# Kernel tuning notes

Hardware: AMD Instinct MI355X
Metric: run time of the kernel (lower is better)

## Reference

```python
import jax, jax.numpy as jnp
import numpy as np
from functools import partial

D_MODEL = 768
N_LAYER = 2
VOCAB = 50264  # 50257 padded to multiple of 8
D_STATE = 16
D_INNER = 2 * D_MODEL
DT_RANK = 48
D_CONV = 4
EPS = 1e-5
ZOH_EPS = 1e-7
B, L = 2, 1024


def setup_inputs() -> dict:
    key = jax.random.key(0)
    ks = jax.random.split(key, 16)
    s = 0.02
    inp = {
        'input_ids': jax.random.randint(ks[0], (B, L), 0, VOCAB, dtype=jnp.int32),
        'embedding': jax.random.normal(ks[1], (VOCAB, D_MODEL), jnp.float32) * s,
        'in_w': jax.random.normal(ks[2], (N_LAYER, D_MODEL, 2 * D_INNER), jnp.float32) * s,
        'in_b': jnp.zeros((N_LAYER, 2 * D_INNER), jnp.float32),
        'conv_w': jax.random.normal(ks[3], (N_LAYER, D_INNER, D_CONV), jnp.float32) * s,
        'conv_b': jnp.zeros((N_LAYER, D_INNER), jnp.float32),
        'xproj_w': jax.random.normal(ks[4], (N_LAYER, D_INNER, DT_RANK + 2 * D_STATE), jnp.float32) * s,
        'dt_w': jax.random.normal(ks[5], (N_LAYER, DT_RANK, D_INNER), jnp.float32) * s,
        'dt_b': jnp.zeros((N_LAYER, D_INNER), jnp.float32),
        'A_log': jnp.broadcast_to(jnp.log(jnp.arange(1, D_STATE + 1, dtype=jnp.float32))[None, None, :], (N_LAYER, D_INNER, D_STATE)).copy(),
        'Dp': jnp.ones((N_LAYER, D_INNER), jnp.float32),
        'out_w': jax.random.normal(ks[6], (N_LAYER, D_INNER, D_MODEL), jnp.float32) * s,
        'out_b': jnp.zeros((N_LAYER, D_MODEL), jnp.float32),
        'norm_w': jnp.ones((N_LAYER, D_MODEL), jnp.float32),
        'normf_w': jnp.ones((D_MODEL,), jnp.float32),
    }
    return inp


def rmsnorm(x, w):
    return x * jax.lax.rsqrt(jnp.mean(x * x, axis=-1, keepdims=True) + EPS) * w


def mamba_block(x, in_w, in_b, conv_w, conv_b, xproj_w, dt_w, dt_b, A_log, Dp, out_w, out_b):
    # x: (b, l, d_model)
    xr = x @ in_w + in_b                       # (b, l, 2*d_inner)
    xi, res = jnp.split(xr, 2, axis=-1)        # each (b, l, d_inner)
    # causal depthwise conv1d (torch pads d_conv-1 both sides then truncates to l)
    xc = jnp.transpose(xi, (0, 2, 1))          # (b, d_inner, l)
    xc = jax.lax.conv_general_dilated(
        xc, conv_w[:, None, :], (1,), [(D_CONV - 1, 0)],
        dimension_numbers=('NCH', 'OIH', 'NCH'), feature_group_count=D_INNER)
    xc = xc + conv_b[None, :, None]
    u = jax.nn.silu(jnp.transpose(xc, (0, 2, 1)))  # (b, l, d_inner)
    res = jax.nn.silu(res)
    # generate time-varying SSM params
    dbc = u @ xproj_w                          # (b, l, dt_rank + 2n)
    dt, Bm, Cm = jnp.split(dbc, [DT_RANK, DT_RANK + D_STATE], axis=-1)
    delta = jax.nn.softplus(dt @ dt_w + dt_b)  # (b, l, d_inner)
    A = -jnp.exp(A_log)                        # (d_inner, n)
    # ZOH discretization
    dA = jnp.exp(jnp.einsum('bld,dn->bldn', delta, A))            # (b,l,d_in,n)
    zoh = (dA - 1.0) / (A + ZOH_EPS)                               # (b,l,d_in,n)
    dBu = zoh * Bm[:, :, None, :] * u[..., None]                   # (b,l,d_in,n)
    # selective scan over l
    def step(s, inputs):
        dA_t, dBu_t, C_t = inputs              # (b,d_in,n),(b,d_in,n),(b,n)
        s = dA_t * s + dBu_t
        y = jnp.einsum('bdn,bn->bd', s, C_t)
        return s, y
    s0 = jnp.zeros((u.shape[0], D_INNER, D_STATE), u.dtype)
    _, ys = jax.lax.scan(step, s0, (jnp.moveaxis(dA, 1, 0), jnp.moveaxis(dBu, 1, 0), jnp.moveaxis(Cm, 1, 0)))
    y = jnp.moveaxis(ys, 0, 1) + u * Dp        # (b, l, d_inner)
    y = y * res
    return y @ out_w + out_b


def forward(input_ids, embedding, in_w, in_b, conv_w, conv_b, xproj_w, dt_w, dt_b, A_log, Dp, out_w, out_b, norm_w, normf_w):
    x = embedding[input_ids]                   # (b, l, d_model)
    for i in range(N_LAYER):
        mixed = mamba_block(x, in_w[i], in_b[i], conv_w[i], conv_b[i], xproj_w[i],
                            dt_w[i], dt_b[i], A_log[i], Dp[i], out_w[i], out_b[i])
        x = rmsnorm(mixed + x, norm_w[i])      # ResidualBlock: norm(mixer(x)+x)
    x = rmsnorm(x, normf_w)
    return x @ embedding.T                     # tied lm_head, (b, l, vocab)


def reference(input_ids, embedding, in_w, in_b, conv_w, conv_b, xproj_w, dt_w, dt_b, A_log, Dp, out_w, out_b, norm_w, normf_w):
    return forward(input_ids, embedding, in_w, in_b, conv_w, conv_b, xproj_w,
                   dt_w, dt_b, A_log, Dp, out_w, out_b, norm_w, normf_w)
```

## Files before the change

### kernel.cpp

```cpp
#include <hip/hip_runtime.h>
#include <math.h>
#include <stdint.h>

#define BB 2
#define LL 1024
#define DM 768
#define NL 2
#define VV 50264
#define VPAD 50304
#define DS 16
#define DI 1536
#define DR 48
#define DC 4
#define MM (BB*LL)

#define CH 32
#define NC (LL/CH)

#define KS 8

#define TS 64
#define KT 16

typedef __attribute__((ext_vector_type(8))) short short8;
typedef __attribute__((ext_vector_type(4))) float f32x4;

#define AS3(p) ((__attribute__((address_space(3))) unsigned int*)(unsigned int)(uintptr_t)(p))
#define AS1(p) ((const __attribute__((address_space(1))) unsigned int*)(uintptr_t)(p))

__device__ __forceinline__ unsigned short f2bf(float v) {
    union { float f; unsigned u; } x; x.f = v;
    unsigned r = x.u + 0x7fffu + ((x.u >> 16) & 1u);
    return (unsigned short)(r >> 16);
}

__global__ __launch_bounds__(256) void embed_kernel(
    const int* __restrict__ ids, const float* __restrict__ emb,
    float* __restrict__ x, unsigned short* __restrict__ x16)
{
    int m = blockIdx.x;
    int v = ids[m];
    const float* src = emb + (size_t)v * DM;
    float* dst = x + (size_t)m * DM;
    unsigned short* dst16 = x16 + (size_t)m * DM;
    for (int i = threadIdx.x; i < DM; i += 256) {
        float f = src[i];
        dst[i] = f;
        dst16[i] = f2bf(f);
    }
}

__global__ __launch_bounds__(256) void emb_convert_kernel(
    const float* __restrict__ emb, unsigned short* __restrict__ out)
{
    size_t i8 = (size_t)blockIdx.x * 256 + threadIdx.x;
    size_t row = i8 / 96;
    size_t col8 = (i8 - row * 96) * 8;
    if (row >= VPAD) return;
    ushort4 o0, o1;
    if (row < VV) {
        const float* p = emb + row * DM + col8;
        float4 v0 = *(const float4*)p;
        float4 v1 = *(const float4*)(p + 4);
        o0.x = f2bf(v0.x); o0.y = f2bf(v0.y); o0.z = f2bf(v0.z); o0.w = f2bf(v0.w);
        o1.x = f2bf(v1.x); o1.y = f2bf(v1.y); o1.z = f2bf(v1.z); o1.w = f2bf(v1.w);
    } else {
        o0 = make_ushort4(0, 0, 0, 0);
        o1 = o0;
    }
    unsigned short* op = out + row * DM + col8;
    *(ushort4*)op = o0;
    *(ushort4*)(op + 4) = o1;
}

__global__ __launch_bounds__(256) void transpose_bf16_kernel(
    const float* __restrict__ in, unsigned short* __restrict__ out, int R, int C)
{
    __shared__ float t[32][33];
    int l = blockIdx.z;
    int r0 = blockIdx.y * 32, c0 = blockIdx.x * 32;
    int tx = threadIdx.x & 31, ty = threadIdx.x >> 5;
    const float* ip = in + (size_t)l * R * C;
    unsigned short* op = out + (size_t)l * C * R;
    #pragma unroll
    for (int j = 0; j < 32; j += 8)
        t[ty + j][tx] = ip[(size_t)(r0 + ty + j) * C + c0 + tx];
    __syncthreads();
    #pragma unroll
    for (int j = 0; j < 32; j += 8)
        op[(size_t)(c0 + ty + j) * R + r0 + tx] = f2bf(t[tx][ty + j]);
}

__global__ __launch_bounds__(256) void gemm_mfma_bt(
    const unsigned short* __restrict__ A, const unsigned short* __restrict__ B,
    const float* __restrict__ bias, const float* __restrict__ resid,
    float* __restrict__ C, int M, int N, int K, int MT, int NTILES)
{
    int T = MT * NTILES;
    int q = T >> 3, r = T & 7;
    int orig = blockIdx.x;
    int xcd = orig & 7, u = orig >> 3;
    int wg = (xcd < r ? xcd * (q + 1) : r * (q + 1) + (xcd - r) * q) + u;
    int mt = wg % MT, nt = wg / MT;

    __shared__ unsigned short As[3][128 * 32];
    __shared__ unsigned short Bs[3][128 * 32];
    int tid = threadIdx.x;
    int w = tid >> 6, lane = tid & 63;
    int m0 = mt * 128, n0 = nt * 128;

    int rA = lane >> 2;
    int kb = (lane & 3) * 8;
    const unsigned short* gA0 = A + (size_t)(m0 + w * 16 + rA) * K + kb;
    const unsigned short* gA1 = gA0 + (size_t)64 * K;
    const unsigned short* gB0 = B + (size_t)(n0 + w * 16 + rA) * K + kb;
    const unsigned short* gB1 = gB0 + (size_t)64 * K;

    int lr = lane & 15, lk = lane >> 4;
    int wr = (w >> 1) * 64, wc = (w & 1) * 64;

    f32x4 acc[4][4] = {};

#define STAGE(k0, buf) do { \
    __builtin_amdgcn_global_load_lds(AS1(gA0 + (k0)), AS3(&As[buf][(w * 16) * 32]), 16, 0, 0); \
    __builtin_amdgcn_global_load_lds(AS1(gA1 + (k0)), AS3(&As[buf][(64 + w * 16) * 32]), 16, 0, 0); \
    __builtin_amdgcn_global_load_lds(AS1(gB0 + (k0)), AS3(&Bs[buf][(w * 16) * 32]), 16, 0, 0); \
    __builtin_amdgcn_global_load_lds(AS1(gB1 + (k0)), AS3(&Bs[buf][(64 + w * 16) * 32]), 16, 0, 0); \
} while (0)

#define COMPUTE(buf) do { \
    short8 a[4], b[4]; \
    _Pragma("unroll") \
    for (int f = 0; f < 4; ++f) \
        a[f] = *(const short8*)&As[buf][(wr + f * 16 + lr) * 32 + lk * 8]; \
    _Pragma("unroll") \
    for (int f = 0; f < 4; ++f) \
        b[f] = *(const short8*)&Bs[buf][(wc + f * 16 + lr) * 32 + lk * 8]; \
    _Pragma("unroll") \
    for (int i = 0; i < 4; ++i) \
        _Pragma("unroll") \
        for (int j = 0; j < 4; ++j) \
            acc[i][j] = __builtin_amdgcn_mfma_f32_16x16x32_bf16(a[i], b[j], acc[i][j], 0, 0, 0); \
} while (0)

    int nsteps = K / 32;
    STAGE(0, 0);
    STAGE(32, 1);
    asm volatile("s_waitcnt vmcnt(4)" ::: "memory");
    __builtin_amdgcn_s_barrier();
    __builtin_amdgcn_sched_barrier(0);

    for (int t = 0; t < nsteps; ++t) {
        int cur = t % 3;
        if (t + 2 < nsteps)
            STAGE((t + 2) * 32, (t + 2) % 3);
        COMPUTE(cur);
        if (t + 1 < nsteps) {
            if (t + 2 < nsteps)
                asm volatile("s_waitcnt vmcnt(4)" ::: "memory");
            else
                asm volatile("s_waitcnt vmcnt(0)" ::: "memory");
            __builtin_amdgcn_s_barrier();
            __builtin_amdgcn_sched_barrier(0);
        }
    }

#undef STAGE
#undef COMPUTE

    #pragma unroll
    for (int i = 0; i < 4; ++i) {
        int row = m0 + wr + i * 16 + lk * 4;
        #pragma unroll
        for (int j = 0; j < 4; ++j) {
            int col = n0 + wc + j * 16 + lr;
            if (col < N) {
                float bv = bias ? bias[col] : 0.f;
                #pragma unroll
                for (int r2 = 0; r2 < 4; ++r2) {
                    float v = acc[i][j][r2] + bv;
                    if (resid) v += resid[(size_t)(row + r2) * N + col];
                    C[(size_t)(row + r2) * N + col] = v;
                }
            }
        }
    }
}

template<int ACT>
__global__ __launch_bounds__(256) void gemm_tiled(
    const float* __restrict__ A, const float* __restrict__ Bm,
    const float* __restrict__ bias, float* __restrict__ C,
    int M, int N, int K, int lda)
{
    __shared__ float As[KT][TS + 4];
    __shared__ float Bs[KT][TS + 4];
    int tid = threadIdx.x;
    int tx = tid & 15, ty = tid >> 4;
    int m0 = blockIdx.y * TS;
    int n0 = blockIdx.x * TS;
    float acc[4][4] = {};

    for (int k0 = 0; k0 < K; k0 += KT) {
        {
            int i = tid >> 2;
            int k4 = (tid & 3) * 4;
            int m = m0 + i;
            float4 v = make_float4(0.f, 0.f, 0.f, 0.f);
            if (m < M) v = *(const float4*)(A + (size_t)m * lda + k0 + k4);
            As[k4 + 0][i] = v.x; As[k4 + 1][i] = v.y;
            As[k4 + 2][i] = v.z; As[k4 + 3][i] = v.w;
        }
        {
            int k = tid >> 4;
            int j4 = (tid & 15) * 4;
            int n = n0 + j4;
            float4 v = make_float4(0.f, 0.f, 0.f, 0.f);
            const float* p = Bm + (size_t)(k0 + k) * N + n;
            if (n + 3 < N) {
                v = *(const float4*)p;
            } else {
                float t0 = (n + 0 < N) ? p[0] : 0.f;
                float t1 = (n + 1 < N) ? p[1] : 0.f;
                float t2 = (n + 2 < N) ? p[2] : 0.f;
                float t3 = (n + 3 < N) ? p[3] : 0.f;
                v = make_float4(t0, t1, t2, t3);
            }
            Bs[k][j4 + 0] = v.x; Bs[k][j4 + 1] = v.y;
            Bs[k][j4 + 2] = v.z; Bs[k][j4 + 3] = v.w;
        }
        __syncthreads();
        #pragma unroll
        for (int k = 0; k < KT; ++k) {
            float a[4], b[4];
            #pragma unroll
            for (int q2 = 0; q2 < 4; ++q2) a[q2] = As[k][ty * 4 + q2];
            #pragma unroll
            for (int q2 = 0; q2 < 4; ++q2) b[q2] = Bs[k][tx * 4 + q2];
            #pragma unroll
            for (int i = 0; i < 4; ++i)
                #pragma unroll
                for (int j = 0; j < 4; ++j)
                    acc[i][j] = fmaf(a[i], b[j], acc[i][j]);
        }
        __syncthreads();
    }

    #pragma unroll
    for (int i = 0; i < 4; ++i) {
        int m = m0 + ty * 4 + i;
        if (m >= M) continue;
        #pragma unroll
        for (int j = 0; j < 4; ++j) {
            int n = n0 + tx * 4 + j;
            if (n >= N) continue;
            float v = acc[i][j];
            if (bias)  v += bias[n];
            if (ACT == 1) v = fmaxf(v, 0.f) + log1pf(expf(-fabsf(v)));
            C[(size_t)m * N + n] = v;
        }
    }
}

__global__ __launch_bounds__(256) void xproj_part_kernel(
    const float* __restrict__ A, const float* __restrict__ Bm, float* __restrict__ part)
{
    __shared__ float As[KT][TS + 4];
    __shared__ float Bs[KT][TS + 4];
    int tid = threadIdx.x;
    int tx = tid & 15, ty = tid >> 4;
    int m0 = blockIdx.y * TS;
    int n0 = blockIdx.x * TS;
    int kbeg = blockIdx.z * (DI / KS);
    const int N = 80;
    float acc[4][4] = {};

    for (int k0 = kbeg; k0 < kbeg + DI / KS; k0 += KT) {
        {
            int i = tid >> 2;
            int k4 = (tid & 3) * 4;
            float4 v = *(const float4*)(A + (size_t)(m0 + i) * DI + k0 + k4);
            As[k4 + 0][i] = v.x; As[k4 + 1][i] = v.y;
            As[k4 + 2][i] = v.z; As[k4 + 3][i] = v.w;
        }
        {
            int k = tid >> 4;
            int j4 = (tid & 15) * 4;
            int n = n0 + j4;
            const float* p = Bm + (size_t)(k0 + k) * N + n;
            float4 v;
            if (n + 3 < N) {
                v = *(const float4*)p;
            } else {
                v.x = (n + 0 < N) ? p[0] : 0.f;
                v.y = (n + 1 < N) ? p[1] : 0.f;
                v.z = (n + 2 < N) ? p[2] : 0.f;
                v.w = (n + 3 < N) ? p[3] : 0.f;
            }
            Bs[k][j4 + 0] = v.x; Bs[k][j4 + 1] = v.y;
            Bs[k][j4 + 2] = v.z; Bs[k][j4 + 3] = v.w;
        }
        __syncthreads();
        #pragma unroll
        for (int k = 0; k < KT; ++k) {
            float a[4], b[4];
            #pragma unroll
            for (int q2 = 0; q2 < 4; ++q2) a[q2] = As[k][ty * 4 + q2];
            #pragma unroll
            for (int q2 = 0; q2 < 4; ++q2) b[q2] = Bs[k][tx * 4 + q2];
            #pragma unroll
            for (int i = 0; i < 4; ++i)
                #pragma unroll
                for (int j = 0; j < 4; ++j)
                    acc[i][j] = fmaf(a[i], b[j], acc[i][j]);
        }
        __syncthreads();
    }

    float* op = part + (size_t)blockIdx.z * MM * 80;
    #pragma unroll
    for (int i = 0; i < 4; ++i) {
        int m = m0 + ty * 4 + i;
        #pragma unroll
        for (int j = 0; j < 4; ++j) {
            int n = n0 + tx * 4 + j;
            if (n < 80) op[(size_t)m * 80 + n] = acc[i][j];
        }
    }
}

__global__ __launch_bounds__(256) void xproj_reduce_kernel(
    const float* __restrict__ part, float* __restrict__ dbc)
{
    int i = blockIdx.x * 256 + threadIdx.x;
    if (i >= MM * 80) return;
    float s = 0.f;
    #pragma unroll
    for (int z = 0; z < KS; ++z) s += part[(size_t)z * MM * 80 + i];
    dbc[i] = s;
}

__global__ __launch_bounds__(256) void conv_silu_kernel(
    const float* __restrict__ xr, const float* __restrict__ cw,
    const float* __restrict__ cb, float* __restrict__ u)
{
    int d = blockIdx.x * 256 + threadIdx.x;
    int l = blockIdx.y;
    int b = blockIdx.z;
    float acc = cb[d];
    #pragma unroll
    for (int j = 0; j < DC; ++j) {
        int lp = l - (DC - 1) + j;
        if (lp >= 0)
            acc = fmaf(xr[((size_t)(b * LL + lp)) * (2 * DI) + d], cw[d * DC + j], acc);
    }
    float s = acc / (1.f + expf(-acc));
    u[((size_t)(b * LL + l)) * DI + d] = s;
}

__global__ __launch_bounds__(256) void scan_reduce_kernel(
    const float* __restrict__ delta, const float* __restrict__ u,
    const float* __restrict__ dbc, const float* __restrict__ A_log,
    float* __restrict__ P, float* __restrict__ Q)
{
    int d = blockIdx.x * 256 + threadIdx.x;
    int c = blockIdx.y;
    int b = blockIdx.z;

    float Av[DS], invA[DS];
    {
        const float4* ap = (const float4*)(A_log + (size_t)d * DS);
        #pragma unroll
        for (int n4 = 0; n4 < 4; ++n4) {
            float4 a = ap[n4];
            Av[n4 * 4 + 0] = -expf(a.x); Av[n4 * 4 + 1] = -expf(a.y);
            Av[n4 * 4 + 2] = -expf(a.z); Av[n4 * 4 + 3] = -expf(a.w);
        }
        #pragma unroll
        for (int n = 0; n < DS; ++n) invA[n] = 1.f / (Av[n] + 1e-7f);
    }

    float p[DS], s[DS];
    #pragma unroll
    for (int n = 0; n < DS; ++n) { p[n] = 1.f; s[n] = 0.f; }

    const float* dp = delta + ((size_t)b * LL + c * CH) * DI + d;
    const float* up = u     + ((size_t)b * LL + c * CH) * DI + d;
    const float* bb = dbc   + ((size_t)b * LL + c * CH) * 80 + DR;

    for (int l = 0; l < CH; ++l) {
        float dlt = dp[(size_t)l * DI];
        float uv  = up[(size_t)l * DI];
        float Bv[DS];
        {
            const float4* bp4 = (const float4*)(bb + (size_t)l * 80);
            #pragma unroll
            for (int n4 = 0; n4 < 4; ++n4) {
                float4 v = bp4[n4];
                Bv[n4 * 4 + 0] = v.x; Bv[n4 * 4 + 1] = v.y;
                Bv[n4 * 4 + 2] = v.z; Bv[n4 * 4 + 3] = v.w;
            }
        }
        #pragma unroll
        for (int n = 0; n < DS; ++n) {
            float dA = expf(dlt * Av[n]);
            float dBu = (dA - 1.f) * invA[n] * Bv[n] * uv;
            p[n] *= dA;
            s[n] = fmaf(dA, s[n], dBu);
        }
    }

    float* Pp = P + (((size_t)b * NC + c) * DI + d) * DS;
    float* Qp = Q + (((size_t)b * NC + c) * DI + d) * DS;
    #pragma unroll
    for (int n4 = 0; n4 < 4; ++n4) {
        ((float4*)Pp)[n4] = make_float4(p[n4 * 4 + 0], p[n4 * 4 + 1], p[n4 * 4 + 2], p[n4 * 4 + 3]);
        ((float4*)Qp)[n4] = make_float4(s[n4 * 4 + 0], s[n4 * 4 + 1], s[n4 * 4 + 2], s[n4 * 4 + 3]);
    }
}

__global__ __launch_bounds__(256) void scan_apply_kernel(
    const float* __restrict__ delta, const float* __restrict__ u,
    const float* __restrict__ dbc, const float* __restrict__ xr,
    const float* __restrict__ A_log, const float* __restrict__ Dp,
    const float* __restrict__ P, const float* __restrict__ Q,
    unsigned short* __restrict__ y16)
{
    int d = blockIdx.x * 256 + threadIdx.x;
    int c = blockIdx.y;
    int b = blockIdx.z;

    float Av[DS], invA[DS];
    {
        const float4* ap = (const float4*)(A_log + (size_t)d * DS);
        #pragma unroll
        for (int n4 = 0; n4 < 4; ++n4) {
            float4 a = ap[n4];
            Av[n4 * 4 + 0] = -expf(a.x); Av[n4 * 4 + 1] = -expf(a.y);
            Av[n4 * 4 + 2] = -expf(a.z); Av[n4 * 4 + 3] = -expf(a.w);
        }
        #pragma unroll
        for (int n = 0; n < DS; ++n) invA[n] = 1.f / (Av[n] + 1e-7f);
    }
    float Dv = Dp[d];

    float s[DS];
    #pragma unroll
    for (int n = 0; n < DS; ++n) s[n] = 0.f;
    for (int cc = 0; cc < c; ++cc) {
        const float* Pp = P + (((size_t)b * NC + cc) * DI + d) * DS;
        const float* Qp = Q + (((size_t)b * NC + cc) * DI + d) * DS;
        float pv[DS], qv[DS];
        #pragma unroll
        for (int n4 = 0; n4 < 4; ++n4) {
            float4 pw = ((const float4*)Pp)[n4];
            float4 qw = ((const float4*)Qp)[n4];
            pv[n4 * 4 + 0] = pw.x; pv[n4 * 4 + 1] = pw.y; pv[n4 * 4 + 2] = pw.z; pv[n4 * 4 + 3] = pw.w;
            qv[n4 * 4 + 0] = qw.x; qv[n4 * 4 + 1] = qw.y; qv[n4 * 4 + 2] = qw.z; qv[n4 * 4 + 3] = qw.w;
        }
        #pragma unroll
        for (int n = 0; n < DS; ++n) s[n] = fmaf(pv[n], s[n], qv[n]);
    }

    const float* dp = delta + ((size_t)b * LL + c * CH) * DI + d;
    const float* up = u     + ((size_t)b * LL + c * CH) * DI + d;
    const float* xp = xr    + ((size_t)b * LL + c * CH) * (2 * DI) + DI + d;
    const float* bb = dbc   + ((size_t)b * LL + c * CH) * 80 + DR;
    unsigned short* yp = y16 + ((size_t)b * LL + c * CH) * DI + d;

    for (int l = 0; l < CH; ++l) {
        float dlt = dp[(size_t)l * DI];
        float uv  = up[(size_t)l * DI];
        float rv  = xp[(size_t)l * (2 * DI)];
        float Bv[DS], Cv[DS];
        {
            const float4* bp4 = (const float4*)(bb + (size_t)l * 80);
            #pragma unroll
            for (int n4 = 0; n4 < 4; ++n4) {
                float4 v = bp4[n4];
                Bv[n4 * 4 + 0] = v.x; Bv[n4 * 4 + 1] = v.y;
                Bv[n4 * 4 + 2] = v.z; Bv[n4 * 4 + 3] = v.w;
            }
            #pragma unroll
            for (int n4 = 0; n4 < 4; ++n4) {
                float4 v = bp4[4 + n4];
                Cv[n4 * 4 + 0] = v.x; Cv[n4 * 4 + 1] = v.y;
                Cv[n4 * 4 + 2] = v.z; Cv[n4 * 4 + 3] = v.w;
            }
        }
        float pv = 0.f;
        #pragma unroll
        for (int n = 0; n < DS; ++n) {
            float dA = expf(dlt * Av[n]);
            float dBu = (dA - 1.f) * invA[n] * Bv[n] * uv;
            s[n] = fmaf(dA, s[n], dBu);
            pv = fmaf(s[n], Cv[n], pv);
        }
        float res = rv / (1.f + expf(-rv));
        yp[(size_t)l * DI] = f2bf((pv + uv * Dv) * res);
    }
}

__global__ __launch_bounds__(256) void rmsnorm_kernel(
    const float* __restrict__ in, const float* __restrict__ w,
    float* __restrict__ outf, unsigned short* __restrict__ outb)
{
    int m = blockIdx.x;
    const float* row = in + (size_t)m * DM;
    float ss = 0.f;
    for (int i = threadIdx.x; i < DM; i += 256) { float v = row[i]; ss = fmaf(v, v, ss); }
    #pragma unroll
    for (int off = 32; off > 0; off >>= 1) ss += __shfl_down(ss, off);
    __shared__ float sred[4];
    __shared__ float sscale;
    int wid = threadIdx.x >> 6;
    if ((threadIdx.x & 63) == 0) sred[wid] = ss;
    __syncthreads();
    if (threadIdx.x == 0) {
        float tot = sred[0] + sred[1] + sred[2] + sred[3];
        sscale = 1.f / sqrtf(tot / (float)DM + 1e-5f);
    }
    __syncthreads();
    float sc = sscale;
    for (int i = threadIdx.x; i < DM; i += 256) {
        float v = row[i] * sc * w[i];
        if (outf) outf[(size_t)m * DM + i] = v;
        if (outb) outb[(size_t)m * DM + i] = f2bf(v);
    }
}

extern "C" void kernel_launch(void* const* d_in, const int* in_sizes, int n_in,
                              void* d_out, int out_size, void* d_ws, size_t ws_size,
                              hipStream_t stream)
{
    const int*   ids      = (const int*)  d_in[0];
    const float* emb      = (const float*)d_in[1];
    const float* in_w     = (const float*)d_in[2];
    const float* in_b     = (const float*)d_in[3];
    const float* conv_w   = (const float*)d_in[4];
    const float* conv_b   = (const float*)d_in[5];
    const float* xproj_w  = (const float*)d_in[6];
    const float* dt_w     = (const float*)d_in[7];
    const float* dt_b     = (const float*)d_in[8];
    const float* A_log    = (const float*)d_in[9];
    const float* Dp       = (const float*)d_in[10];
    const float* out_w    = (const float*)d_in[11];
    const float* out_b    = (const float*)d_in[12];
    const float* norm_w   = (const float*)d_in[13];
    const float* normf_w  = (const float*)d_in[14];
    float* out = (float*)d_out;

    char* wsp = (char*)d_ws;
    auto alloc = [&](size_t bytes) {
        char* p = wsp;
        wsp += (bytes + 255) & ~(size_t)255;
        return p;
    };
    float* x     = (float*)alloc((size_t)MM * DM * 4);
    float* xr    = (float*)alloc((size_t)MM * 2 * DI * 4);
    float* u     = (float*)alloc((size_t)MM * DI * 4);
    float* dbc   = (float*)alloc((size_t)MM * 80 * 4);
    float* part  = (float*)alloc((size_t)KS * MM * 80 * 4);
    float* delta = (float*)alloc((size_t)MM * DI * 4);
    float* tmp   = (float*)alloc((size_t)MM * DM * 4);
    float* Pbuf  = (float*)alloc((size_t)BB * NC * DI * DS * 4);
    float* Qbuf  = (float*)alloc((size_t)BB * NC * DI * DS * 4);
    unsigned short* x16     = (unsigned short*)alloc((size_t)MM * DM * 2);
    unsigned short* y16     = (unsigned short*)alloc((size_t)MM * DI * 2);
    unsigned short* emb16   = (unsigned short*)alloc((size_t)VPAD * DM * 2);
    unsigned short* in_wT   = (unsigned short*)alloc((size_t)NL * 2 * DI * DM * 2);
    unsigned short* out_wT  = (unsigned short*)alloc((size_t)NL * DM * DI * 2);

    emb_convert_kernel<<<(VPAD * (DM / 8) + 255) / 256, 256, 0, stream>>>(emb, emb16);
    transpose_bf16_kernel<<<dim3(2 * DI / 32, DM / 32, NL), 256, 0, stream>>>(
        in_w, in_wT, DM, 2 * DI);
    transpose_bf16_kernel<<<dim3(DM / 32, DI / 32, NL), 256, 0, stream>>>(
        out_w, out_wT, DI, DM);

    embed_kernel<<<MM, 256, 0, stream>>>(ids, emb, x, x16);

    for (int layer = 0; layer < NL; ++layer) {
        const float* lb_in  = in_b    + (size_t)layer * 2 * DI;
        const float* lcw    = conv_w  + (size_t)layer * DI * DC;
        const float* lcb    = conv_b  + (size_t)layer * DI;
        const float* lxw    = xproj_w + (size_t)layer * DI * (DR + 2 * DS);
        const float* ldtw   = dt_w    + (size_t)layer * DR * DI;
        const float* ldtb   = dt_b    + (size_t)layer * DI;
        const float* lAlog  = A_log   + (size_t)layer * DI * DS;
        const float* lDp    = Dp      + (size_t)layer * DI;
        const float* lob    = out_b   + (size_t)layer * DM;
        const float* lnw    = norm_w  + (size_t)layer * DM;
        const unsigned short* lw_inT = in_wT  + (size_t)layer * 2 * DI * DM;
        const unsigned short* lw_outT= out_wT + (size_t)layer * DM * DI;

        gemm_mfma_bt<<<16 * 24, 256, 0, stream>>>(
            x16, lw_inT, lb_in, nullptr, xr, MM, 2 * DI, DM, 16, 24);

        conv_silu_kernel<<<dim3(DI / 256, LL, BB), 256, 0, stream>>>(xr, lcw, lcb, u);

        xproj_part_kernel<<<dim3(2, MM / TS, KS), 256, 0, stream>>>(u, lxw, part);
        xproj_reduce_kernel<<<(MM * 80 + 255) / 256, 256, 0, stream>>>(part, dbc);

        gemm_tiled<1><<<dim3(DI / TS, MM / TS), 256, 0, stream>>>(
            dbc, ldtw, ldtb, delta, MM, DI, DR, DR + 2 * DS);

        scan_reduce_kernel<<<dim3(DI / 256, NC, BB), 256, 0, stream>>>(
            delta, u, dbc, lAlog, Pbuf, Qbuf);
        scan_apply_kernel<<<dim3(DI / 256, NC, BB), 256, 0, stream>>>(
            delta, u, dbc, xr, lAlog, lDp, Pbuf, Qbuf, y16);

        gemm_mfma_bt<<<16 * 6, 256, 0, stream>>>(
            y16, lw_outT, lob, x, tmp, MM, DM, DI, 16, 6);

        rmsnorm_kernel<<<MM, 256, 0, stream>>>(tmp, lnw, x, x16);
    }

    rmsnorm_kernel<<<MM, 256, 0, stream>>>(x, normf_w, nullptr, x16);

    gemm_mfma_bt<<<16 * (VPAD / 128), 256, 0, stream>>>(
        x16, emb16, nullptr, nullptr, out, MM, VV, DM, 16, VPAD / 128);
}
```

Before: 861.8 us.

## Use a 256x256-tile triple-buffered MFMA GEMM for the tied LM head

Adds a dedicated bf16 MFMA GEMM for the vocabulary projection. It uses 256x256 output tiles, 512 threads, triple-buffered direct global-to-LDS loads, split A/B staging interleaved with compute, XCD-aware block remapping and raised scheduling priority around the MFMAs. The vocabulary padding grows to a multiple of 256 to fit the larger tile. The aim is more data reuse per loaded byte and better overlap in the dominant logits GEMM. In exchange the kernel uses more LDS and registers, which may lower occupancy, and the padded tile count increases slightly.

```diff
diff --git a/kernel.cpp b/kernel.cpp
--- a/kernel.cpp
+++ b/kernel.cpp
@@ -7,7 +7,7 @@
 #define DM 768
 #define NL 2
 #define VV 50264
-#define VPAD 50304
+#define VP2 50432
 #define DS 16
 #define DI 1536
 #define DR 48
@@ -56,7 +56,7 @@
     size_t i8 = (size_t)blockIdx.x * 256 + threadIdx.x;
     size_t row = i8 / 96;
     size_t col8 = (i8 - row * 96) * 8;
-    if (row >= VPAD) return;
+    if (row >= VP2) return;
     ushort4 o0, o1;
     if (row < VV) {
         const float* p = emb + row * DM + col8;
@@ -182,6 +182,121 @@
                     if (resid) v += resid[(size_t)(row + r2) * N + col];
                     C[(size_t)(row + r2) * N + col] = v;
                 }
+            }
+        }
+    }
+}
+
+__global__ __launch_bounds__(512) void gemm_mfma_256(
+    const unsigned short* __restrict__ A, const unsigned short* __restrict__ B,
+    float* __restrict__ C, int M, int N, int K, int MT, int NTILES)
+{
+    int T = MT * NTILES;
+    int q = T >> 3, r = T & 7;
+    int orig = blockIdx.x;
+    int xcd = orig & 7, u = orig >> 3;
+    int wg = (xcd < r ? xcd * (q + 1) : r * (q + 1) + (xcd - r) * q) + u;
+    int mt = wg % MT, nt = wg / MT;
+
+    __shared__ unsigned short As[3][256 * 32];
+    __shared__ unsigned short Bs[3][256 * 32];
+    int tid = threadIdx.x;
+    int w = tid >> 6, lane = tid & 63;
+    int wm = w >> 2, wn = w & 3;
+    int m0 = mt * 256, n0 = nt * 256;
+
+    int srow = tid >> 2;
+    int schunk = (tid & 3) ^ ((srow & 3) ^ ((srow >> 2) & 3));
+    const unsigned short* gA0 = A + (size_t)(m0 + srow) * K + schunk * 8;
+    const unsigned short* gA1 = gA0 + (size_t)128 * K;
+    const unsigned short* gB0 = B + (size_t)(n0 + srow) * K + schunk * 8;
+    const unsigned short* gB1 = gB0 + (size_t)128 * K;
+
+    int lr = lane & 15, lk = lane >> 4;
+    int rc = (lk ^ ((lr & 3) ^ ((lr >> 2) & 3))) * 8;
+
+    f32x4 acc[8][4] = {};
+
+#define STAGE_A(k0, buf) do { \
+    __builtin_amdgcn_global_load_lds(AS1(gA0 + (k0)), AS3(&As[buf][(w * 16) * 32]), 16, 0, 0); \
+    __builtin_amdgcn_global_load_lds(AS1(gA1 + (k0)), AS3(&As[buf][(128 + w * 16) * 32]), 16, 0, 0); \
+} while (0)
+#define STAGE_B(k0, buf) do { \
+    __builtin_amdgcn_global_load_lds(AS1(gB0 + (k0)), AS3(&Bs[buf][(w * 16) * 32]), 16, 0, 0); \
+    __builtin_amdgcn_global_load_lds(AS1(gB1 + (k0)), AS3(&Bs[buf][(128 + w * 16) * 32]), 16, 0, 0); \
+} while (0)
+
+    int nsteps = K / 32;
+
+    STAGE_A(0, 0); STAGE_B(0, 0);
+    STAGE_A(32, 1); STAGE_B(32, 1);
+    asm volatile("s_waitcnt vmcnt(4)" ::: "memory");
+    __builtin_amdgcn_s_barrier();
+    __builtin_amdgcn_sched_barrier(0);
+
+    for (int t = 0; t < nsteps; ++t) {
+        int s = t % 3;
+        int sn = (t + 2) % 3;
+        bool stage2 = (t + 2) < nsteps;
+        short8 av[4], bv[4];
+
+        #pragma unroll
+        for (int f = 0; f < 4; ++f)
+            av[f] = *(const short8*)&As[s][(wm * 128 + f * 16 + lr) * 32 + rc];
+        #pragma unroll
+        for (int f = 0; f < 4; ++f)
+            bv[f] = *(const short8*)&Bs[s][(wn * 64 + f * 16 + lr) * 32 + rc];
+        if (stage2) STAGE_A((t + 2) * 32, sn);
+        __builtin_amdgcn_s_barrier();
+        asm volatile("s_waitcnt lgkmcnt(0)" ::: "memory");
+        __builtin_amdgcn_sched_barrier(0);
+        __builtin_amdgcn_s_setprio(1);
+        #pragma unroll
+        for (int i = 0; i < 4; ++i)
+            #pragma unroll
+            for (int j = 0; j < 4; ++j)
+                acc[i][j] = __builtin_amdgcn_mfma_f32_16x16x32_bf16(av[i], bv[j], acc[i][j], 0, 0, 0);
+        __builtin_amdgcn_s_setprio(0);
+        __builtin_amdgcn_s_barrier();
+
+        #pragma unroll
+        for (int f = 0; f < 4; ++f)
+            av[f] = *(const short8*)&As[s][(wm * 128 + (4 + f) * 16 + lr) * 32 + rc];
+        if (stage2) STAGE_B((t + 2) * 32, sn);
+        __builtin_amdgcn_s_barrier();
+        asm volatile("s_waitcnt lgkmcnt(0)" ::: "memory");
+        __builtin_amdgcn_sched_barrier(0);
+        __builtin_amdgcn_s_setprio(1);
+        #pragma unroll
+        for (int i = 0; i < 4; ++i)
+            #pragma unroll
+            for (int j = 0; j < 4; ++j)
+                acc[4 + i][j] = __builtin_amdgcn_mfma_f32_16x16x32_bf16(av[i], bv[j], acc[4 + i][j], 0, 0, 0);
+        __builtin_amdgcn_s_setprio(0);
+
+        if (t + 1 < nsteps) {
+            if (stage2)
+                asm volatile("s_waitcnt vmcnt(4)" ::: "memory");
+            else
+                asm volatile("s_waitcnt vmcnt(0)" ::: "memory");
+            __builtin_amdgcn_s_barrier();
+            __builtin_amdgcn_sched_barrier(0);
+        }
+    }
+
+#undef STAGE_A
+#undef STAGE_B
+
+    #pragma unroll
+    for (int i = 0; i < 8; ++i) {
+        int row = m0 + wm * 128 + i * 16 + lk * 4;
+        #pragma unroll
+        for (int j = 0; j < 4; ++j) {
+            int col = n0 + wn * 64 + j * 16 + lr;
+            if (col < N) {
+                #pragma unroll
+                for (int r2 = 0; r2 < 4; ++r2)
+                    C[(size_t)(row + r2) * N + col] = acc[i][j][r2];
             }
         }
     }
@@ -567,11 +682,11 @@
     float* Qbuf  = (float*)alloc((size_t)BB * NC * DI * DS * 4);
     unsigned short* x16     = (unsigned short*)alloc((size_t)MM * DM * 2);
     unsigned short* y16     = (unsigned short*)alloc((size_t)MM * DI * 2);
-    unsigned short* emb16   = (unsigned short*)alloc((size_t)VPAD * DM * 2);
+    unsigned short* emb16   = (unsigned short*)alloc((size_t)VP2 * DM * 2);
     unsigned short* in_wT   = (unsigned short*)alloc((size_t)NL * 2 * DI * DM * 2);
     unsigned short* out_wT  = (unsigned short*)alloc((size_t)NL * DM * DI * 2);
 
-    emb_convert_kernel<<<(VPAD * (DM / 8) + 255) / 256, 256, 0, stream>>>(emb, emb16);
+    emb_convert_kernel<<<((size_t)VP2 * (DM / 8) + 255) / 256, 256, 0, stream>>>(emb, emb16);
     transpose_bf16_kernel<<<dim3(2 * DI / 32, DM / 32, NL), 256, 0, stream>>>(
         in_w, in_wT, DM, 2 * DI);
     transpose_bf16_kernel<<<dim3(DM / 32, DI / 32, NL), 256, 0, stream>>>(
@@ -617,6 +732,6 @@
 
     rmsnorm_kernel<<<MM, 256, 0, stream>>>(x, normf_w, nullptr, x16);
 
-    gemm_mfma_bt<<<16 * (VPAD / 128), 256, 0, stream>>>(
-        x16, emb16, nullptr, nullptr, out, MM, VV, DM, 16, VPAD / 128);
-}
+    gemm_mfma_256<<<8 * (VP2 / 256), 512, 0, stream>>>(
+        x16, emb16, out, MM, VV, DM, 8, VP2 / 256);
+}
```

Result: faster. 810.9 us (-5.9%).
